# Kernel optimization log

Measured on AMD Instinct MI355X. Metric: run time of the kernel, lower is better.

The kernel has to match this reference:

```python
import jax, jax.numpy as jnp
import numpy as np

B, C, OC, H, W = 2, 64, 128, 96, 96
HD, DI, N, R, K = C // 2, C, 16, 2, 4  # VSSBlock: hidden=C/2, d_inner=2*hidden=C, d_state, dt_rank, 4 scan dirs
EPS = 1e-5


def _conv(x, w, b, pad, groups=1):
    y = jax.lax.conv_general_dilated(x, w, (1, 1), pad, feature_group_count=groups,
                                     dimension_numbers=('NCHW', 'OIHW', 'NCHW'))
    return y + b[None, :, None, None]


def _ln(x, w, b):
    m = x.mean(-1, keepdims=True)
    v = x.var(-1, keepdims=True)
    return (x - m) * jax.lax.rsqrt(v + EPS) * w + b


def _selective_scan(xs, dts, Bs, Cs, A, D):
    # xs, dts: (B,K,DI,L); Bs, Cs: (B,K,N,L); A: (K,DI,N); D: (K,DI)
    dts = jax.nn.softplus(dts)

    def step(h, inp):
        u_t, dt_t, B_t, C_t = inp
        dA = jnp.exp(dt_t[..., None] * A)                         # (B,K,DI,N)
        h = dA * h + (dt_t * u_t)[..., None] * B_t[:, :, None, :]
        return h, jnp.einsum('bkdn,bkn->bkd', h, C_t)

    seq = (jnp.moveaxis(xs, -1, 0), jnp.moveaxis(dts, -1, 0),
           jnp.moveaxis(Bs, -1, 0), jnp.moveaxis(Cs, -1, 0))
    h0 = jnp.zeros(xs.shape[:3] + (A.shape[-1],), xs.dtype)
    _, ys = jax.lax.scan(step, h0, seq)
    return jnp.moveaxis(ys, 0, -1) + D[None, :, :, None] * xs


def _vss_block(x, ln_w, ln_b, in_w, conv_w, conv_b, xproj_w, dtproj_w, dtproj_b,
               A_logs, Ds, on_w, on_b, out_w):
    # x: (B,H,W,HD); VMamba SS2D with 4-direction cross-scan + residual
    b, hh, ww, _ = x.shape
    L = hh * ww
    h = _ln(x, ln_w, ln_b)
    xz = h @ in_w                                   # (B,H,W,2*DI)
    xp, z = jnp.split(xz, 2, axis=-1)
    xc = jnp.transpose(xp, (0, 3, 1, 2))            # (B,DI,H,W)
    xc = jax.nn.silu(_conv(xc, conv_w, conv_b, ((1, 1), (1, 1)), groups=DI))
    x_flat = xc.reshape(b, DI, L)
    x_wh = jnp.transpose(xc, (0, 1, 3, 2)).reshape(b, DI, L)
    x2 = jnp.stack([x_flat, x_wh], axis=1)
    xs = jnp.concatenate([x2, jnp.flip(x2, -1)], axis=1)      # (B,4,DI,L)
    x_dbl = jnp.einsum('bkdl,kcd->bkcl', xs, xproj_w)
    dts, Bs, Cs = jnp.split(x_dbl, [R, R + N], axis=2)
    dts = jnp.einsum('bkrl,kdr->bkdl', dts, dtproj_w) + dtproj_b[None, :, :, None]
    A = -jnp.exp(A_logs)
    ys = _selective_scan(xs, dts, Bs, Cs, A, Ds)              # (B,4,DI,L)
    inv = jnp.flip(ys[:, 2:4], -1)
    unwh = lambda t: jnp.transpose(t.reshape(b, DI, ww, hh), (0, 1, 3, 2)).reshape(b, DI, L)
    y = ys[:, 0] + inv[:, 0] + unwh(ys[:, 1]) + unwh(inv[:, 1])
    y = jnp.transpose(y.reshape(b, DI, hh, ww), (0, 2, 3, 1))
    y = _ln(y, on_w, on_b) * jax.nn.silu(z)
    return x + y @ out_w


def _forward(x, ms_dw33_w, ms_dw33_b, ms_in_w, ms_in_b, ms_scale,
             vss_ln_w, vss_ln_b, vss_in_w, vss_conv_w, vss_conv_b, vss_xproj_w,
             vss_dtproj_w, vss_dtproj_b, vss_A_logs, vss_Ds, vss_on_w, vss_on_b, vss_out_w,
             ma_conv_w, ma_conv_b, adw_h_w, adw_h_b, adw_w_w, adw_w_b,
             pw_w, pw_b, bn_w, bn_b, bn_mean, bn_var):
    vss = (vss_ln_w, vss_ln_b, vss_in_w, vss_conv_w, vss_conv_b, vss_xproj_w,
           vss_dtproj_w, vss_dtproj_b, vss_A_logs, vss_Ds, vss_on_w, vss_on_b, vss_out_w)
    # --- MambaSplit (shared VSSBlock applied to both channel halves) ---
    xd = _conv(x, ms_dw33_w, ms_dw33_b, ((1, 1), (1, 1)), groups=C)
    x1, x2 = jnp.split(xd, 2, axis=1)

    def branch(xp):
        y = _vss_block(jnp.transpose(xp, (0, 2, 3, 1)), *vss)
        return ms_scale * xp + jnp.transpose(y, (0, 3, 1, 2))

    xm = jnp.concatenate([branch(x1), branch(x2)], axis=1)
    m = xm.mean((2, 3), keepdims=True)
    v = xm.var((2, 3), keepdims=True)
    xm = (xm - m) * jax.lax.rsqrt(v + EPS) * ms_in_w[None, :, None, None] + ms_in_b[None, :, None, None]
    xm = jax.nn.leaky_relu(xm, 0.01)
    # --- MaxAvg (global avg+max pool -> 3x3 conv on 1x1 map -> sigmoid gate) ---
    pooled = jnp.concatenate([x.mean((2, 3), keepdims=True), x.max((2, 3), keepdims=True)], axis=1)
    gate = jax.nn.sigmoid(_conv(pooled, ma_conv_w, ma_conv_b, ((1, 1), (1, 1))))
    xs_ = xm + gate * x
    # --- AxialDW ---
    xs_ = xs_ + _conv(xs_, adw_h_w, adw_h_b, ((1, 1), (0, 0)), groups=C) \
              + _conv(xs_, adw_w_w, adw_w_b, ((0, 0), (1, 1)), groups=C)
    # --- BN (eval) + ReLU, 1x1 conv, 2x2 maxpool ---
    skip = jax.nn.relu((xs_ - bn_mean[None, :, None, None]) * jax.lax.rsqrt(bn_var[None, :, None, None] + EPS)
                       * bn_w[None, :, None, None] + bn_b[None, :, None, None])
    out = _conv(skip, pw_w, pw_b, ((0, 0), (0, 0)))
    down = jax.lax.reduce_window(out, -jnp.inf, jax.lax.max, (1, 1, 2, 2), (1, 1, 2, 2), 'VALID')
    return down, skip


def setup_inputs() -> dict:
    key = jax.random.key(0)
    ks = jax.random.split(key, 16)
    r = lambda i, shape, s=0.02: jax.random.normal(ks[i], shape, jnp.float32) * s
    return {
        'x': jax.random.normal(ks[0], (B, C, H, W), jnp.float32),
        'ms_dw33_w': r(1, (C, 1, 3, 3), 0.1), 'ms_dw33_b': jnp.zeros(C),
        'ms_in_w': jnp.ones(C), 'ms_in_b': jnp.zeros(C),
        'ms_scale': jnp.ones((1,)),
        'vss_ln_w': jnp.ones(HD), 'vss_ln_b': jnp.zeros(HD),
        'vss_in_w': r(2, (HD, 2 * DI)),
        'vss_conv_w': r(3, (DI, 1, 3, 3), 0.1), 'vss_conv_b': jnp.zeros(DI),
        'vss_xproj_w': r(4, (K, R + 2 * N, DI)),
        'vss_dtproj_w': r(5, (K, DI, R), 0.1), 'vss_dtproj_b': r(6, (K, DI), 0.1),
        'vss_A_logs': jnp.tile(jnp.log(jnp.arange(1, N + 1, dtype=jnp.float32)), (K, DI, 1)),
        'vss_Ds': jnp.ones((K, DI)),
        'vss_on_w': jnp.ones(DI), 'vss_on_b': jnp.zeros(DI),
        'vss_out_w': r(7, (DI, HD)),
        'ma_conv_w': r(8, (C, 2 * C, 3, 3), 0.05), 'ma_conv_b': jnp.zeros(C),
        'adw_h_w': r(9, (C, 1, 3, 1), 0.1), 'adw_h_b': jnp.zeros(C),
        'adw_w_w': r(10, (C, 1, 1, 3), 0.1), 'adw_w_b': jnp.zeros(C),
        'pw_w': r(11, (OC, C, 1, 1)), 'pw_b': jnp.zeros(OC),
        'bn_w': jnp.ones(C), 'bn_b': jnp.zeros(C),
        'bn_mean': jnp.zeros(C), 'bn_var': jnp.ones(C),
    }


def reference(x, ms_dw33_w, ms_dw33_b, ms_in_w, ms_in_b, ms_scale,
              vss_ln_w, vss_ln_b, vss_in_w, vss_conv_w, vss_conv_b, vss_xproj_w,
              vss_dtproj_w, vss_dtproj_b, vss_A_logs, vss_Ds, vss_on_w, vss_on_b, vss_out_w,
              ma_conv_w, ma_conv_b, adw_h_w, adw_h_b, adw_w_w, adw_w_b,
              pw_w, pw_b, bn_w, bn_b, bn_mean, bn_var):
    return _forward(x, ms_dw33_w, ms_dw33_b, ms_in_w, ms_in_b, ms_scale,
                    vss_ln_w, vss_ln_b, vss_in_w, vss_conv_w, vss_conv_b, vss_xproj_w,
                    vss_dtproj_w, vss_dtproj_b, vss_A_logs, vss_Ds, vss_on_w, vss_on_b, vss_out_w,
                    ma_conv_w, ma_conv_b, adw_h_w, adw_h_b, adw_w_w, adw_w_b,
                    pw_w, pw_b, bn_w, bn_b, bn_mean, bn_var)
```

## Files before the change

kernel.cpp:

```cpp
#include <hip/hip_runtime.h>
#include <hip/hip_bf16.h>

typedef __hip_bfloat16 bf16;
#define DEV __device__ __forceinline__

constexpr int B_ = 2, C_ = 64, H_ = 96, W_ = 96, L_ = 9216;
constexpr int HD_ = 32, DI_ = 64, N_ = 16, K_ = 4, BB_ = 4;
constexpr int OC_ = 128;
constexpr int CH_ = 768, CL_ = 12;
constexpr int SEGN = 16, SEGC = 48;
constexpr float EPSF = 1e-5f;
constexpr int DOWN_SZ = B_ * OC_ * 48 * 48;

typedef __attribute__((ext_vector_type(8))) short short8;
typedef __attribute__((ext_vector_type(4))) float f32x4;

DEV float softplusf(float x) { return x > 15.f ? x : __logf(1.f + __expf(x)); }
DEV float b2f(bf16 v) { return __bfloat162float(v); }
DEV float lo16f(unsigned v) { return __uint_as_float(v << 16); }
DEV float hi16f(unsigned v) { return __uint_as_float(v & 0xffff0000u); }
DEV void unpk(uint4 a, uint4 b, float* v) {
  v[0] = lo16f(a.x); v[1] = hi16f(a.x); v[2] = lo16f(a.y); v[3] = hi16f(a.y);
  v[4] = lo16f(a.z); v[5] = hi16f(a.z); v[6] = lo16f(a.w); v[7] = hi16f(a.w);
  v[8] = lo16f(b.x); v[9] = hi16f(b.x); v[10] = lo16f(b.y); v[11] = hi16f(b.y);
  v[12] = lo16f(b.z); v[13] = hi16f(b.z); v[14] = lo16f(b.w); v[15] = hi16f(b.w);
}

__constant__ float kLogN[16] = {
  0.0f, 0.69314718f, 1.09861229f, 1.38629436f, 1.60943791f, 1.79175947f,
  1.94591015f, 2.07944154f, 2.19722458f, 2.30258509f, 2.39789527f,
  2.48490665f, 2.56494936f, 2.63905733f, 2.70805020f, 2.77258872f};

DEV void pow_tree(float e1, float* ep) {
  float e2 = e1 * e1, e4 = e2 * e2, e8 = e4 * e4;
  float e3 = e2 * e1, e5 = e4 * e1, e6 = e4 * e2, e7 = e4 * e3;
  ep[0] = e1;  ep[1] = e2;  ep[2] = e3;  ep[3] = e4;
  ep[4] = e5;  ep[5] = e6;  ep[6] = e7;  ep[7] = e8;
  ep[8] = e8 * e1;  ep[9] = e8 * e2;  ep[10] = e8 * e3;  ep[11] = e8 * e4;
  ep[12] = e8 * e5; ep[13] = e8 * e6; ep[14] = e8 * e7;  ep[15] = e8 * e8;
}

DEV void ld_bu(const float* __restrict__ bB, const bf16* __restrict__ ub, int d,
               int ls, int uidx, uint4& qb0, uint4& qb1, float& t0, float& t1, float& u) {
  int uls = __builtin_amdgcn_readfirstlane(ls);
  const float* p = bB + (size_t)uls * 12;
  qb0 = *(const uint4*)p; qb1 = *(const uint4*)(p + 4);
  t0 = p[8]; t1 = p[9];
  u = b2f(ub[(size_t)uidx * DI_ + d]);
}
DEV void ld_bcu(const float* __restrict__ bB, const bf16* __restrict__ bC,
                const bf16* __restrict__ ub, int d, int ls, int uidx,
                uint4& qb0, uint4& qb1, uint4& qc0, uint4& qc1,
                float& t0, float& t1, float& u) {
  int uls = __builtin_amdgcn_readfirstlane(ls);
  const float* p = bB + (size_t)uls * 12;
  qb0 = *(const uint4*)p; qb1 = *(const uint4*)(p + 4);
  t0 = p[8]; t1 = p[9];
  const uint4* cq = (const uint4*)(bC + (size_t)uls * 16);
  qc0 = cq[0]; qc1 = cq[1];
  u = b2f(ub[(size_t)uidx * DI_ + d]);
}

__global__ void k_dw33(const float* __restrict__ x, const float* __restrict__ w,
                       const float* __restrict__ bias, float* __restrict__ out) {
  int t = blockIdx.x * 256 + threadIdx.x;
  if (t >= B_ * C_ * L_) return;
  int wi = t % W_, hi = (t / W_) % H_, c = (t / L_) % C_;
  float acc = bias[c];
#pragma unroll
  for (int dy = -1; dy <= 1; dy++) {
    int hh = hi + dy; if (hh < 0 || hh >= H_) continue;
#pragma unroll
    for (int dx = -1; dx <= 1; dx++) {
      int ww = wi + dx; if (ww < 0 || ww >= W_) continue;
      acc = fmaf(x[t + dy * W_ + dx], w[c * 9 + (dy + 1) * 3 + (dx + 1)], acc);
    }
  }
  out[t] = acc;
}

__global__ __launch_bounds__(256, 4) void k_ln_inproj(
    const float* __restrict__ xd, const float* __restrict__ lnw,
    const float* __restrict__ lnb, const float* __restrict__ inw,
    float* __restrict__ xzA, bf16* __restrict__ xzBh) {
  int bb = blockIdx.y, t = threadIdx.x;
  int b = bb & 1, co = (bb >> 1) * HD_;
  int idx0 = blockIdx.x * 64;
  __shared__ float xds[32 * 68];
  __shared__ float meanA[64], rstdA[64];
  int lane = t & 63;
  for (int r = 0; r < 8; r++) {
    int c = r * 4 + (t >> 6);
    xds[c * 68 + lane] = xd[(size_t)(b * C_ + co + c) * L_ + idx0 + lane];
  }
  __syncthreads();
  if (t < 64) {
    float s = 0.f, sq = 0.f;
#pragma unroll
    for (int c = 0; c < 32; c++) { float v = xds[c * 68 + t]; s += v; sq = fmaf(v, v, sq); }
    float mean = s * (1.f / HD_);
    float var = sq * (1.f / HD_) - mean * mean;
    meanA[t] = mean; rstdA[t] = rsqrtf(var + EPSF);
  }
  __syncthreads();
  for (int i = t; i < 2048; i += 256) {
    int c = i >> 6, idx = i & 63;
    float v = xds[c * 68 + idx];
    xds[c * 68 + idx] = (v - meanA[idx]) * rstdA[idx] * lnw[c] + lnb[c];
  }
  __syncthreads();
  int oc = t & 127, g = t >> 7;
  float acc[32];
#pragma unroll
  for (int j = 0; j < 32; j++) acc[j] = 0.f;
  for (int c = 0; c < 32; c++) {
    float wv = inw[c * 128 + oc];
    const float4* row = reinterpret_cast<const float4*>(&xds[c * 68 + g * 32]);
#pragma unroll
    for (int j4 = 0; j4 < 8; j4++) {
      float4 xv = row[j4];
      acc[j4 * 4 + 0] = fmaf(xv.x, wv, acc[j4 * 4 + 0]);
      acc[j4 * 4 + 1] = fmaf(xv.y, wv, acc[j4 * 4 + 1]);
      acc[j4 * 4 + 2] = fmaf(xv.z, wv, acc[j4 * 4 + 2]);
      acc[j4 * 4 + 3] = fmaf(xv.w, wv, acc[j4 * 4 + 3]);
    }
  }
  int occ = oc & 63;
  if (oc < 64) {
#pragma unroll
    for (int j = 0; j < 32; j++)
      xzA[(size_t)(bb * L_ + idx0 + g * 32 + j) * 64 + occ] = acc[j];
  } else {
#pragma unroll
    for (int j = 0; j < 32; j++)
      xzBh[(size_t)(bb * L_ + idx0 + g * 32 + j) * 64 + occ] = __float2bfloat16(acc[j]);
  }
}

__global__ void k_dwsilu(const float* __restrict__ xzA, const float* __restrict__ cw,
                         const float* __restrict__ cb, bf16* __restrict__ xch,
                         bf16* __restrict__ xcht) {
  int t = blockIdx.x * 256 + threadIdx.x;
  int d = t & 63, idx = (t >> 6) % L_, bb = t / (L_ * DI_);
  int wi = idx % W_, hi = idx / W_;
  float acc = cb[d];
#pragma unroll
  for (int dy = -1; dy <= 1; dy++) {
    int hh = hi + dy; if (hh < 0 || hh >= H_) continue;
#pragma unroll
    for (int dx = -1; dx <= 1; dx++) {
      int ww = wi + dx; if (ww < 0 || ww >= W_) continue;
      acc = fmaf(xzA[(size_t)(bb * L_ + hh * W_ + ww) * 64 + d],
                 cw[d * 9 + (dy + 1) * 3 + (dx + 1)], acc);
    }
  }
  acc = acc / (1.f + __expf(-acc));
  bf16 v = __float2bfloat16(acc);
  xch[t] = v;
  int idx_t = wi * 96 + hi;
  xcht[((size_t)bb * L_ + idx_t) * DI_ + d] = v;
}

__global__ void k_wprep(const float* __restrict__ xpw, const float* __restrict__ alog,
                        bf16* __restrict__ wh, float* __restrict__ aux) {
  int i = blockIdx.x * 256 + threadIdx.x;
  if (i < 144 * 64) {
    int n = i >> 6;
    wh[i] = __float2bfloat16(n < 136 ? xpw[i] : 0.f);
  }
  if (blockIdx.x == 0 && threadIdx.x < 256) {
    int kd = threadIdx.x;
    const float* al = alog + kd * N_;
    float a0 = al[0];
    bool lin = true;
#pragma unroll
    for (int n = 1; n < N_; n++) lin = lin && (fabsf(al[n] - a0 - kLogN[n]) < 3e-5f);
    aux[kd] = -__expf(a0);
    aux[256 + kd] = lin ? 1.f : 0.f;
#pragma unroll
    for (int n = 0; n < N_; n++) aux[512 + kd * N_ + n] = -__expf(al[n]);
  }
}

__global__ __launch_bounds__(256, 4) void k_xdbl_mfma(
    const bf16* __restrict__ xch, const bf16* __restrict__ wh,
    float* __restrict__ xdblB, bf16* __restrict__ xdblC) {
  int w = threadIdx.x >> 6, lane = threadIdx.x & 63;
  int bb = blockIdx.y;
  int mtile = blockIdx.x * 4 + w;
  int idx0 = mtile * 16;
  int m = lane & 15, quad = lane >> 4;
  const bf16* arow = xch + ((size_t)bb * L_ + idx0 + m) * 64 + quad * 8;
  short8 a0 = *reinterpret_cast<const short8*>(arow);
  short8 a1 = *reinterpret_cast<const short8*>(arow + 32);
#pragma unroll
  for (int nt = 0; nt < 9; nt++) {
    int n = nt * 16 + m;
    const bf16* brow = wh + n * 64 + quad * 8;
    short8 b0 = *reinterpret_cast<const short8*>(brow);
    short8 b1 = *reinterpret_cast<const short8*>(brow + 32);
    f32x4 acc = {0.f, 0.f, 0.f, 0.f};
    acc = __builtin_amdgcn_mfma_f32_16x16x32_bf16(a0, b0, acc, 0, 0, 0);
    acc = __builtin_amdgcn_mfma_f32_16x16x32_bf16(a1, b1, acc, 0, 0, 0);
    if (n < 136) {
      int k4 = (n >= 102) ? 3 : (n >= 68) ? 2 : (n >= 34) ? 1 : 0;
      int c = n - k4 * 34;
#pragma unroll
      for (int i = 0; i < 4; i++) {
        int r = idx0 + quad * 4 + i;
        int hi2 = r / 96, wi2 = r - hi2 * 96;
        int tr = wi2 * 96 + hi2;
        int ls = (k4 == 0) ? r : (k4 == 1) ? tr : (k4 == 2) ? (L_ - 1 - r) : (L_ - 1 - tr);
        size_t row = (size_t)(bb * K_ + k4) * L_ + ls;
        if (c < 2)       xdblB[row * 12 + 8 + c] = acc[i];
        else if (c < 18) ((bf16*)(xdblB + row * 12))[c - 2] = __float2bfloat16(acc[i]);
        else             xdblC[row * 16 + (c - 18)] = __float2bfloat16(acc[i]);
      }
    }
  }
}

__global__ __launch_bounds__(256, 4) void k_scan1(
    const float* __restrict__ xdblB, const bf16* __restrict__ xch,
    const bf16* __restrict__ xcht, const float* __restrict__ dtw,
    const float* __restrict__ dtb, const float* __restrict__ aux,
    bf16* __restrict__ hbuf, float* __restrict__ ssum) {
  int w = threadIdx.x >> 6, d = threadIdx.x & 63;
  int chunk = blockIdx.x * 4 + w, k = blockIdx.y, bb = blockIdx.z;
  float w0 = dtw[(k * DI_ + d) * 2 + 0], w1 = dtw[(k * DI_ + d) * 2 + 1];
  float bia = dtb[k * DI_ + d];
  float A1 = aux[k * 64 + d];
  bool chain = (__ballot(aux[256 + k * 64 + d] > 0.5f) == ~0ull);
  float h[N_];
#pragma unroll
  for (int n = 0; n < N_; n++) h[n] = 0.f;
  const float* bB = xdblB + (size_t)(bb * K_ + k) * L_ * 12;
  const bf16* ub = ((k & 1) ? xcht : xch) + (size_t)bb * L_ * DI_;
  int ls0 = chunk * CL_;
  int uidx0 = (k & 2) ? (L_ - 1 - ls0) : ls0;
  int ustep = (k & 2) ? -1 : 1;
  float S = 0.f;
  if (chain) {
#pragma unroll 2
    for (int s = 0; s < CL_; s++) {
      uint4 qb0, qb1; float t0, t1, u;
      ld_bu(bB, ub, d, ls0 + s, uidx0 + s * ustep, qb0, qb1, t0, t1, u);
      float Bv[16];
      unpk(qb0, qb1, Bv);
      float dt = softplusf(fmaf(t0, w0, fmaf(t1, w1, bia)));
      S += dt;
      float du = dt * u;
      float ep[16];
      pow_tree(__expf(dt * A1), ep);
#pragma unroll
      for (int n = 0; n < N_; n++) h[n] = fmaf(ep[n], h[n], du * Bv[n]);
    }
  } else {
    float A[N_];
#pragma unroll
    for (int n = 0; n < N_; n++) A[n] = aux[512 + (k * 64 + d) * N_ + n];
    for (int s = 0; s < CL_; s++) {
      uint4 qb0, qb1; float t0, t1, u;
      ld_bu(bB, ub, d, ls0 + s, uidx0 + s * ustep, qb0, qb1, t0, t1, u);
      float Bv[16];
      unpk(qb0, qb1, Bv);
      float dt = softplusf(fmaf(t0, w0, fmaf(t1, w1, bia)));
      S += dt;
      float du = dt * u;
#pragma unroll
      for (int n = 0; n < N_; n++) h[n] = fmaf(__expf(dt * A[n]), h[n], du * Bv[n]);
    }
  }
  size_t base = (size_t)((bb * K_ + k) * CH_ + chunk) * DI_ + d;
  ssum[base] = S;
#pragma unroll
  for (int n = 0; n < N_; n++) hbuf[base * N_ + n] = __float2bfloat16(h[n]);
}

__global__ __launch_bounds__(256, 4) void k_scan2a(
    const float* __restrict__ aux, const float* __restrict__ ssum,
    bf16* __restrict__ hbuf, float* __restrict__ cumS,
    float* __restrict__ segH, float* __restrict__ segS) {
  int t = blockIdx.x * 256 + threadIdx.x;
  int n = t & 15, d = (t >> 4) & 63, kk = (t >> 10) & 3, bb = (t >> 12) & 3, seg = t >> 14;
  float A = aux[512 + (kk * 64 + d) * N_ + n];
  size_t row = (size_t)(bb * K_ + kk) * CH_ * DI_ + d;
  float hp = 0.f, Sc = 0.f;
#pragma unroll 4
  for (int j = 0; j < SEGC; j++) {
    int c = seg * SEGC + j;
    size_t sb = row + (size_t)c * DI_;
    float S = ssum[sb];
    float hl = b2f(hbuf[sb * N_ + n]);
    hbuf[sb * N_ + n] = __float2bfloat16(hp);
    if (n == 0) cumS[sb] = Sc;
    hp = fmaf(__expf(A * S), hp, hl);
    Sc += S;
  }
  size_t sbase = (size_t)(bb * K_ + kk) * SEGN + seg;
  segH[(sbase * DI_ + d) * N_ + n] = hp;
  if (n == 0) segS[sbase * DI_ + d] = Sc;
}

__global__ void k_scan2b(const float* __restrict__ aux, float* __restrict__ segH,
                         const float* __restrict__ segS) {
  int t = blockIdx.x * 256 + threadIdx.x;
  int n = t & 15, d = (t >> 4) & 63, kk = (t >> 10) & 3, bb = t >> 12;
  float A = aux[512 + (kk * 64 + d) * N_ + n];
  float hp = 0.f;
  for (int seg = 0; seg < SEGN; seg++) {
    size_t sbase = (size_t)(bb * K_ + kk) * SEGN + seg;
    size_t si = (sbase * DI_ + d) * N_ + n;
    float H = segH[si];
    float E = __expf(A * segS[sbase * DI_ + d]);
    segH[si] = hp;
    hp = fmaf(E, hp, H);
  }
}

__global__ __launch_bounds__(256, 4) void k_scan3(
    const float* __restrict__ xdblB, const bf16* __restrict__ xdblC,
    const bf16* __restrict__ xch, const bf16* __restrict__ xcht,
    const float* __restrict__ dtw, const float* __restrict__ dtb,
    const float* __restrict__ Dsw, const float* __restrict__ aux,
    const bf16* __restrict__ hbuf, const float* __restrict__ cumS,
    const float* __restrict__ segH, bf16* __restrict__ ydir) {
  int w = threadIdx.x >> 6, d = threadIdx.x & 63;
  int chunk = blockIdx.x * 4 + w, k = blockIdx.y, bb = blockIdx.z;
  float w0 = dtw[(k * DI_ + d) * 2 + 0], w1 = dtw[(k * DI_ + d) * 2 + 1];
  float bia = dtb[k * DI_ + d];
  float Dk = Dsw[k * DI_ + d];
  float A1 = aux[k * 64 + d];
  bool chain = (__ballot(aux[256 + k * 64 + d] > 0.5f) == ~0ull);
  float h[N_];
  size_t base = (size_t)((bb * K_ + k) * CH_ + chunk) * DI_ + d;
  int seg = chunk / SEGC;
  size_t sbase = (size_t)(bb * K_ + k) * SEGN + seg;
  float Sc = cumS[base];
  {
    const bf16* hb = hbuf + base * N_;
    uint4 qh0 = *(const uint4*)hb, qh1 = *(const uint4*)(hb + 8);
    unpk(qh0, qh1, h);
    const float* Hin = segH + (sbase * DI_ + d) * N_;
    if (chain) {
      float ep[16];
      pow_tree(__expf(A1 * Sc), ep);
#pragma unroll
      for (int n = 0; n < N_; n++) h[n] = fmaf(ep[n], Hin[n], h[n]);
    } else {
#pragma unroll
      for (int n = 0; n < N_; n++) {
        float A = aux[512 + (k * 64 + d) * N_ + n];
        h[n] = fmaf(__expf(A * Sc), Hin[n], h[n]);
      }
    }
  }
  const float* bB = xdblB + (size_t)(bb * K_ + k) * L_ * 12;
  const bf16* bC = xdblC + (size_t)(bb * K_ + k) * L_ * 16;
  const bf16* ub = ((k & 1) ? xcht : xch) + (size_t)bb * L_ * DI_;
  bf16* yb = ydir + (size_t)(bb * K_ + k) * L_ * DI_;
  int ls0 = chunk * CL_;
  int uidx0 = (k & 2) ? (L_ - 1 - ls0) : ls0;
  int ustep = (k & 2) ? -1 : 1;
  if (chain) {
#pragma unroll 2
    for (int s = 0; s < CL_; s++) {
      uint4 qb0, qb1, qc0, qc1; float t0, t1, u;
      ld_bcu(bB, bC, ub, d, ls0 + s, uidx0 + s * ustep, qb0, qb1, qc0, qc1, t0, t1, u);
      float Bv[16], Cv[16];
      unpk(qb0, qb1, Bv); unpk(qc0, qc1, Cv);
      float dt = softplusf(fmaf(t0, w0, fmaf(t1, w1, bia)));
      float du = dt * u;
      float ep[16];
      pow_tree(__expf(dt * A1), ep);
      float m[16];
#pragma unroll
      for (int n = 0; n < N_; n++) {
        h[n] = fmaf(ep[n], h[n], du * Bv[n]);
        m[n] = h[n] * Cv[n];
      }
      float a0 = m[0] + m[1], a1 = m[2] + m[3], a2 = m[4] + m[5], a3 = m[6] + m[7];
      float a4 = m[8] + m[9], a5 = m[10] + m[11], a6 = m[12] + m[13], a7 = m[14] + m[15];
      float b0 = a0 + a1, b1 = a2 + a3, b2 = a4 + a5, b3 = a6 + a7;
      float y = fmaf(Dk, u, (b0 + b1) + (b2 + b3));
      yb[(size_t)(ls0 + s) * DI_ + d] = __float2bfloat16(y);
    }
  } else {
    float A[N_];
#pragma unroll
    for (int n = 0; n < N_; n++) A[n] = aux[512 + (k * 64 + d) * N_ + n];
    for (int s = 0; s < CL_; s++) {
      uint4 qb0, qb1, qc0, qc1; float t0, t1, u;
      ld_bcu(bB, bC, ub, d, ls0 + s, uidx0 + s * ustep, qb0, qb1, qc0, qc1, t0, t1, u);
      float Bv[16], Cv[16];
      unpk(qb0, qb1, Bv); unpk(qc0, qc1, Cv);
      float dt = softplusf(fmaf(t0, w0, fmaf(t1, w1, bia)));
      float du = dt * u;
      float y = 0.f;
#pragma unroll
      for (int n = 0; n < N_; n++) {
        h[n] = fmaf(__expf(dt * A[n]), h[n], du * Bv[n]);
        y = fmaf(h[n], Cv[n], y);
      }
      y = fmaf(Dk, u, y);
      yb[(size_t)(ls0 + s) * DI_ + d] = __float2bfloat16(y);
    }
  }
}

__global__ void k_combine(const bf16* __restrict__ ydir, const bf16* __restrict__ xzBh,
                          const float* __restrict__ xd, const float* __restrict__ onw,
                          const float* __restrict__ onb, const float* __restrict__ outw,
                          const float* __restrict__ mssc, float* __restrict__ xm) {
  int w = threadIdx.x >> 6, d = threadIdx.x & 63;
  int idx = blockIdx.x * 4 + w, bb = blockIdx.y;
  int b = bb & 1, co = (bb >> 1) * HD_;
  int hii = idx / 96, wii = idx - hii * 96;
  int lt = wii * 96 + hii;
  const bf16* yd = ydir + (size_t)bb * K_ * L_ * DI_;
  float y = b2f(yd[((size_t)0 * L_ + idx) * DI_ + d])
          + b2f(yd[((size_t)1 * L_ + lt) * DI_ + d])
          + b2f(yd[((size_t)2 * L_ + (L_ - 1 - idx)) * DI_ + d])
          + b2f(yd[((size_t)3 * L_ + (L_ - 1 - lt)) * DI_ + d]);
  float s = y, sq = y * y;
#pragma unroll
  for (int m = 1; m < 64; m <<= 1) { s += __shfl_xor(s, m, 64); sq += __shfl_xor(sq, m, 64); }
  float mean = s * (1.f / DI_);
  float var = sq * (1.f / DI_) - mean * mean;
  float rstd = rsqrtf(var + EPSF);
  float yn = (y - mean) * rstd * onw[d] + onb[d];
  float z = b2f(xzBh[(size_t)(bb * L_ + idx) * 64 + d]);
  float g = yn * (z / (1.f + __expf(-z)));
  __shared__ float gs[4][DI_];
  gs[w][d] = g;
  __syncthreads();
  if (d < HD_) {
    float acc = 0.f;
#pragma unroll
    for (int dd = 0; dd < DI_; dd++) acc = fmaf(gs[w][dd], outw[dd * HD_ + d], acc);
    size_t xi = (size_t)(b * C_ + co + d) * L_ + idx;
    float xp = xd[xi];
    xm[xi] = mssc[0] * xp + xp + acc;
  }
}

__global__ __launch_bounds__(1024) void k_stats(
    const float* __restrict__ xm, const float* __restrict__ x,
    float* __restrict__ inm, float* __restrict__ inr,
    float* __restrict__ xmean, float* __restrict__ xmax) {
  int bc = blockIdx.x, t = threadIdx.x;
  const float* pm = xm + (size_t)bc * L_;
  const float* px = x + (size_t)bc * L_;
  float s = 0.f, sq = 0.f, xs = 0.f, mx = -1e30f;
  for (int i = t; i < L_; i += 1024) {
    float v = pm[i]; s += v; sq = fmaf(v, v, sq);
    float xv = px[i]; xs += xv; mx = fmaxf(mx, xv);
  }
  __shared__ float red[64];
#pragma unroll
  for (int m = 1; m < 64; m <<= 1) {
    s += __shfl_xor(s, m, 64); sq += __shfl_xor(sq, m, 64);
    xs += __shfl_xor(xs, m, 64); mx = fmaxf(mx, __shfl_xor(mx, m, 64));
  }
  int wid = t >> 6;
  if ((t & 63) == 0) { red[wid] = s; red[16 + wid] = sq; red[32 + wid] = xs; red[48 + wid] = mx; }
  __syncthreads();
  if (t == 0) {
    s = 0.f; sq = 0.f; xs = 0.f; mx = -1e30f;
#pragma unroll
    for (int i = 0; i < 16; i++) {
      s += red[i]; sq += red[16 + i]; xs += red[32 + i]; mx = fmaxf(mx, red[48 + i]);
    }
    float mean = s * (1.f / L_);
    float var = sq * (1.f / L_) - mean * mean;
    inm[bc] = mean;
    inr[bc] = rsqrtf(var + EPSF);
    xmean[bc] = xs * (1.f / L_);
    xmax[bc] = mx;
  }
}

__global__ void k_xs(const float* __restrict__ xm, const float* __restrict__ inm,
                     const float* __restrict__ inr, const float* __restrict__ msw,
                     const float* __restrict__ msb, const float* __restrict__ xmean,
                     const float* __restrict__ xmax, const float* __restrict__ maw,
                     const float* __restrict__ mab, const float* __restrict__ x,
                     float* __restrict__ xs2) {
  int t = blockIdx.x * 256 + threadIdx.x;
  int bc = t / L_, c = bc & 63, b = bc >> 6;
  __shared__ float gsh;
  if (threadIdx.x < 64) {
    int ic = threadIdx.x;
    float p = xmean[b * 64 + ic] * maw[(c * 128 + ic) * 9 + 4]
            + xmax[b * 64 + ic] * maw[(c * 128 + 64 + ic) * 9 + 4];
#pragma unroll
    for (int m = 1; m < 64; m <<= 1) p += __shfl_xor(p, m, 64);
    if (ic == 0) gsh = 1.f / (1.f + __expf(-(p + mab[c])));
  }
  __syncthreads();
  float gate = gsh;
  float v = xm[t];
  v = (v - inm[bc]) * inr[bc] * msw[c] + msb[c];
  v = v > 0.f ? v : 0.01f * v;
  xs2[t] = v + gate * x[t];
}

__global__ void k_axbn(const float* __restrict__ xs2, const float* __restrict__ hw,
                       const float* __restrict__ hb, const float* __restrict__ wwt,
                       const float* __restrict__ wb, const float* __restrict__ bnw,
                       const float* __restrict__ bnb, const float* __restrict__ bnm,
                       const float* __restrict__ bnv, float* __restrict__ skipo) {
  int t = blockIdx.x * 256 + threadIdx.x;
  if (t >= B_ * C_ * L_) return;
  int wi = t % W_, hi = (t / W_) % H_, c = (t / L_) % C_;
  float a = xs2[t];
  float hacc = hb[c];
#pragma unroll
  for (int dy = -1; dy <= 1; dy++) {
    int hh = hi + dy; if (hh < 0 || hh >= H_) continue;
    hacc = fmaf(xs2[t + dy * W_], hw[c * 3 + dy + 1], hacc);
  }
  float wacc = wb[c];
#pragma unroll
  for (int dx = -1; dx <= 1; dx++) {
    int ww = wi + dx; if (ww < 0 || ww >= W_) continue;
    wacc = fmaf(xs2[t + dx], wwt[c * 3 + dx + 1], wacc);
  }
  float v = a + hacc + wacc;
  float sv = (v - bnm[c]) * rsqrtf(bnv[c] + EPSF) * bnw[c] + bnb[c];
  skipo[t] = fmaxf(sv, 0.f);
}

__global__ void k_pwpool(const float* __restrict__ skipo, const float* __restrict__ pww,
                         const float* __restrict__ pwb, float* __restrict__ down) {
  int h2 = blockIdx.x, b = blockIdx.y, t = threadIdx.x;
  int oc0 = blockIdx.z * 32;
  __shared__ float sk[64 * 192];
  for (int i = t; i < 64 * 192; i += 256) {
    int c = i / 192, rw = i % 192, r = rw / 96, wcol = rw % 96;
    sk[i] = skipo[((size_t)(b * C_ + c) * H_ + (2 * h2 + r)) * W_ + wcol];
  }
  __syncthreads();
  for (int o = t; o < 32 * 48; o += 256) {
    int oc = oc0 + o / 48, w2 = o % 48;
    float s0 = 0.f, s1 = 0.f, s2 = 0.f, s3 = 0.f;
#pragma unroll 8
    for (int c = 0; c < 64; c++) {
      float wv = pww[oc * 64 + c];
      const float* sp = &sk[c * 192 + 2 * w2];
      s0 = fmaf(sp[0], wv, s0);
      s1 = fmaf(sp[1], wv, s1);
      s2 = fmaf(sp[96], wv, s2);
      s3 = fmaf(sp[97], wv, s3);
    }
    float v = fmaxf(fmaxf(s0, s1), fmaxf(s2, s3)) + pwb[oc];
    down[((size_t)(b * OC_ + oc) * 48 + h2) * 48 + w2] = v;
  }
}

extern "C" void kernel_launch(void* const* d_in, const int* in_sizes, int n_in,
                              void* d_out, int out_size, void* d_ws, size_t ws_size,
                              hipStream_t stream) {
  const float* x     = (const float*)d_in[0];
  const float* dw33w = (const float*)d_in[1];
  const float* dw33b = (const float*)d_in[2];
  const float* msw   = (const float*)d_in[3];
  const float* msb   = (const float*)d_in[4];
  const float* mssc  = (const float*)d_in[5];
  const float* lnw   = (const float*)d_in[6];
  const float* lnb   = (const float*)d_in[7];
  const float* inw   = (const float*)d_in[8];
  const float* cw    = (const float*)d_in[9];
  const float* cb    = (const float*)d_in[10];
  const float* xpw   = (const float*)d_in[11];
  const float* dtw   = (const float*)d_in[12];
  const float* dtb   = (const float*)d_in[13];
  const float* alog  = (const float*)d_in[14];
  const float* Dsw   = (const float*)d_in[15];
  const float* onw   = (const float*)d_in[16];
  const float* onb   = (const float*)d_in[17];
  const float* outw  = (const float*)d_in[18];
  const float* maw   = (const float*)d_in[19];
  const float* mab   = (const float*)d_in[20];
  const float* ahw   = (const float*)d_in[21];
  const float* ahb   = (const float*)d_in[22];
  const float* aww   = (const float*)d_in[23];
  const float* awb   = (const float*)d_in[24];
  const float* pww   = (const float*)d_in[25];
  const float* pwb   = (const float*)d_in[26];
  const float* bnw   = (const float*)d_in[27];
  const float* bnb   = (const float*)d_in[28];
  const float* bnm   = (const float*)d_in[29];
  const float* bnv   = (const float*)d_in[30];

  float* ws = (float*)d_ws;
  float* xd    = ws;
  float* hreg  = xd + 1179648;
  bf16*  hbuf  = (bf16*)hreg;
  float* xzA   = hreg;
  bf16*  xzBh  = (bf16*)(hreg + 6291456);
  float* xdblB = hreg + 6291456 + 1179648;
  bf16*  xdblC = (bf16*)(xdblB + 1769472);
  float* ssum  = xdblB + 1769472 + 1179648;
  bf16*  ydir  = (bf16*)(ssum + 786432);
  float* xmR   = ssum + 786432 + 4718592;
  bf16*  xch   = (bf16*)xmR;
  float* xm    = xmR;
  float* xs2   = (float*)ydir;
  float* st    = xmR + 1179648;
  float* inm = st, *inr = st + 128, *xmean = st + 256, *xmaxv = st + 384;
  float* aux   = st + 512;
  bf16*  wh    = (bf16*)(aux + 4608);
  float* cumS  = aux + 4608 + 4608;
  float* segH  = cumS + 786432;
  float* segS  = segH + 262144;
  bf16*  xcht  = (bf16*)(segS + 16384);

  float* outp = (float*)d_out;
  float* down = outp;
  float* skipo = outp + DOWN_SZ;

  dim3 b256(256);
  int nEl = B_ * C_ * L_;

  k_wprep<<<dim3(36), b256, 0, stream>>>(xpw, alog, wh, aux);
  k_dw33<<<dim3((nEl + 255) / 256), b256, 0, stream>>>(x, dw33w, dw33b, xd);
  k_ln_inproj<<<dim3(L_ / 64, BB_), b256, 0, stream>>>(xd, lnw, lnb, inw, xzA, xzBh);
  k_dwsilu<<<dim3(BB_ * L_ * DI_ / 256), b256, 0, stream>>>(xzA, cw, cb, xch, xcht);
  k_xdbl_mfma<<<dim3(L_ / 64, BB_), b256, 0, stream>>>(xch, wh, xdblB, xdblC);
  k_scan1<<<dim3(CH_ / 4, K_, BB_), b256, 0, stream>>>(xdblB, xch, xcht, dtw, dtb, aux, hbuf, ssum);
  k_scan2a<<<dim3(BB_ * K_ * SEGN * DI_ * N_ / 256), b256, 0, stream>>>(aux, ssum, hbuf, cumS, segH, segS);
  k_scan2b<<<dim3(BB_ * K_ * DI_ * N_ / 256), b256, 0, stream>>>(aux, segH, segS);
  k_scan3<<<dim3(CH_ / 4, K_, BB_), b256, 0, stream>>>(xdblB, xdblC, xch, xcht, dtw, dtb, Dsw,
                                                      aux, hbuf, cumS, segH, ydir);
  k_combine<<<dim3(L_ / 4, BB_), b256, 0, stream>>>(ydir, xzBh, xd, onw, onb, outw, mssc, xm);
  k_stats<<<dim3(B_ * C_), dim3(1024), 0, stream>>>(xm, x, inm, inr, xmean, xmaxv);
  k_xs<<<dim3((nEl + 255) / 256), b256, 0, stream>>>(xm, inm, inr, msw, msb, xmean, xmaxv, maw, mab, x, xs2);
  k_axbn<<<dim3((nEl + 255) / 256), b256, 0, stream>>>(xs2, ahw, ahb, aww, awb, bnw, bnb, bnm, bnv, skipo);
  k_pwpool<<<dim3(48, B_, 4), b256, 0, stream>>>(skipo, pww, pwb, down);
}
```

Baseline: 320.7 us.

## Fuse front-end kernels, fold segment-carry scan into scan3, merge xs into axbn

Merges weight prep, the depthwise 3x3 conv and LayerNorm+in-proj into a single front kernel that computes the conv directly into shared memory. Removes the separate cross-segment scan kernel by having each scan3 thread recompute its segment-prefix state from segH/segS. Fuses the xs computation into the axial-conv+BN kernel, recomputing neighbour values instead of round-tripping xs2 through memory. Intent is fewer launches and less intermediate global traffic, at the cost of redundant recomputation.

```diff
diff --git a/kernel.cpp b/kernel.cpp
--- a/kernel.cpp
+++ b/kernel.cpp
@@ -61,37 +61,54 @@
   u = b2f(ub[(size_t)uidx * DI_ + d]);
 }
 
-__global__ void k_dw33(const float* __restrict__ x, const float* __restrict__ w,
-                       const float* __restrict__ bias, float* __restrict__ out) {
-  int t = blockIdx.x * 256 + threadIdx.x;
-  if (t >= B_ * C_ * L_) return;
-  int wi = t % W_, hi = (t / W_) % H_, c = (t / L_) % C_;
-  float acc = bias[c];
-#pragma unroll
-  for (int dy = -1; dy <= 1; dy++) {
-    int hh = hi + dy; if (hh < 0 || hh >= H_) continue;
-#pragma unroll
-    for (int dx = -1; dx <= 1; dx++) {
-      int ww = wi + dx; if (ww < 0 || ww >= W_) continue;
-      acc = fmaf(x[t + dy * W_ + dx], w[c * 9 + (dy + 1) * 3 + (dx + 1)], acc);
-    }
-  }
-  out[t] = acc;
-}
-
-__global__ __launch_bounds__(256, 4) void k_ln_inproj(
-    const float* __restrict__ xd, const float* __restrict__ lnw,
+__global__ __launch_bounds__(256, 4) void k_front(
+    const float* __restrict__ x, const float* __restrict__ dw33w,
+    const float* __restrict__ dw33b, const float* __restrict__ lnw,
     const float* __restrict__ lnb, const float* __restrict__ inw,
-    float* __restrict__ xzA, bf16* __restrict__ xzBh) {
+    const float* __restrict__ xpw, const float* __restrict__ alog,
+    float* __restrict__ xd, float* __restrict__ xzA, bf16* __restrict__ xzBh,
+    bf16* __restrict__ wh, float* __restrict__ aux) {
   int bb = blockIdx.y, t = threadIdx.x;
   int b = bb & 1, co = (bb >> 1) * HD_;
   int idx0 = blockIdx.x * 64;
+  if (bb == 0) {
+    int i = blockIdx.x * 256 + t;
+    if (i < 144 * 64) {
+      int n = i >> 6;
+      wh[i] = __float2bfloat16(n < 136 ? xpw[i] : 0.f);
+    }
+    if (blockIdx.x == 0) {
+      int kd = t;
+      const float* al = alog + kd * N_;
+      float a0 = al[0];
+      bool lin = true;
+#pragma unroll
+      for (int n = 1; n < N_; n++) lin = lin && (fabsf(al[n] - a0 - kLogN[n]) < 3e-5f);
+      aux[kd] = -__expf(a0);
+      aux[256 + kd] = lin ? 1.f : 0.f;
+#pragma unroll
+      for (int n = 0; n < N_; n++) aux[512 + kd * N_ + n] = -__expf(al[n]);
+    }
+  }
   __shared__ float xds[32 * 68];
   __shared__ float meanA[64], rstdA[64];
-  int lane = t & 63;
-  for (int r = 0; r < 8; r++) {
-    int c = r * 4 + (t >> 6);
-    xds[c * 68 + lane] = xd[(size_t)(b * C_ + co + c) * L_ + idx0 + lane];
+  for (int i = t; i < 2048; i += 256) {
+    int cl = i >> 6, ii = i & 63;
+    int sp = idx0 + ii, wi = sp % 96, hi = sp / 96;
+    int cg = b * C_ + co + cl;
+    float acc = dw33b[co + cl];
+#pragma unroll
+    for (int dy = -1; dy <= 1; dy++) {
+      int hh = hi + dy; if (hh < 0 || hh >= H_) continue;
+#pragma unroll
+      for (int dx = -1; dx <= 1; dx++) {
+        int ww = wi + dx; if (ww < 0 || ww >= W_) continue;
+        acc = fmaf(x[(size_t)cg * L_ + sp + dy * 96 + dx],
+                   dw33w[(co + cl) * 9 + (dy + 1) * 3 + (dx + 1)], acc);
+      }
+    }
+    xds[cl * 68 + ii] = acc;
+    xd[(size_t)cg * L_ + sp] = acc;
   }
   __syncthreads();
   if (t < 64) {
@@ -159,27 +176,6 @@
   xch[t] = v;
   int idx_t = wi * 96 + hi;
   xcht[((size_t)bb * L_ + idx_t) * DI_ + d] = v;
-}
-
-__global__ void k_wprep(const float* __restrict__ xpw, const float* __restrict__ alog,
-                        bf16* __restrict__ wh, float* __restrict__ aux) {
-  int i = blockIdx.x * 256 + threadIdx.x;
-  if (i < 144 * 64) {
-    int n = i >> 6;
-    wh[i] = __float2bfloat16(n < 136 ? xpw[i] : 0.f);
-  }
-  if (blockIdx.x == 0 && threadIdx.x < 256) {
-    int kd = threadIdx.x;
-    const float* al = alog + kd * N_;
-    float a0 = al[0];
-    bool lin = true;
-#pragma unroll
-    for (int n = 1; n < N_; n++) lin = lin && (fabsf(al[n] - a0 - kLogN[n]) < 3e-5f);
-    aux[kd] = -__expf(a0);
-    aux[256 + kd] = lin ? 1.f : 0.f;
-#pragma unroll
-    for (int n = 0; n < N_; n++) aux[512 + kd * N_ + n] = -__expf(al[n]);
-  }
 }
 
 __global__ __launch_bounds__(256, 4) void k_xdbl_mfma(
@@ -302,29 +298,14 @@
   if (n == 0) segS[sbase * DI_ + d] = Sc;
 }
 
-__global__ void k_scan2b(const float* __restrict__ aux, float* __restrict__ segH,
-                         const float* __restrict__ segS) {
-  int t = blockIdx.x * 256 + threadIdx.x;
-  int n = t & 15, d = (t >> 4) & 63, kk = (t >> 10) & 3, bb = t >> 12;
-  float A = aux[512 + (kk * 64 + d) * N_ + n];
-  float hp = 0.f;
-  for (int seg = 0; seg < SEGN; seg++) {
-    size_t sbase = (size_t)(bb * K_ + kk) * SEGN + seg;
-    size_t si = (sbase * DI_ + d) * N_ + n;
-    float H = segH[si];
-    float E = __expf(A * segS[sbase * DI_ + d]);
-    segH[si] = hp;
-    hp = fmaf(E, hp, H);
-  }
-}
-
 __global__ __launch_bounds__(256, 4) void k_scan3(
     const float* __restrict__ xdblB, const bf16* __restrict__ xdblC,
     const bf16* __restrict__ xch, const bf16* __restrict__ xcht,
     const float* __restrict__ dtw, const float* __restrict__ dtb,
     const float* __restrict__ Dsw, const float* __restrict__ aux,
     const bf16* __restrict__ hbuf, const float* __restrict__ cumS,
-    const float* __restrict__ segH, bf16* __restrict__ ydir) {
+    const float* __restrict__ segH, const float* __restrict__ segS,
+    bf16* __restrict__ ydir) {
   int w = threadIdx.x >> 6, d = threadIdx.x & 63;
   int chunk = blockIdx.x * 4 + w, k = blockIdx.y, bb = blockIdx.z;
   float w0 = dtw[(k * DI_ + d) * 2 + 0], w1 = dtw[(k * DI_ + d) * 2 + 1];
@@ -332,27 +313,44 @@
   float Dk = Dsw[k * DI_ + d];
   float A1 = aux[k * 64 + d];
   bool chain = (__ballot(aux[256 + k * 64 + d] > 0.5f) == ~0ull);
+  float A[N_];
+  if (!chain) {
+#pragma unroll
+    for (int n = 0; n < N_; n++) A[n] = aux[512 + (k * 64 + d) * N_ + n];
+  }
+  int seg = chunk / SEGC;
+  float Hi[N_];
+#pragma unroll
+  for (int n = 0; n < N_; n++) Hi[n] = 0.f;
+  for (int s = 0; s < seg; s++) {
+    size_t sb = (size_t)(bb * K_ + k) * SEGN + s;
+    float Ssg = segS[sb * DI_ + d];
+    const float* Hs = segH + (sb * DI_ + d) * N_;
+    if (chain) {
+      float ep[16];
+      pow_tree(__expf(A1 * Ssg), ep);
+#pragma unroll
+      for (int n = 0; n < N_; n++) Hi[n] = fmaf(ep[n], Hi[n], Hs[n]);
+    } else {
+#pragma unroll
+      for (int n = 0; n < N_; n++) Hi[n] = fmaf(__expf(A[n] * Ssg), Hi[n], Hs[n]);
+    }
+  }
   float h[N_];
   size_t base = (size_t)((bb * K_ + k) * CH_ + chunk) * DI_ + d;
-  int seg = chunk / SEGC;
-  size_t sbase = (size_t)(bb * K_ + k) * SEGN + seg;
   float Sc = cumS[base];
   {
     const bf16* hb = hbuf + base * N_;
     uint4 qh0 = *(const uint4*)hb, qh1 = *(const uint4*)(hb + 8);
     unpk(qh0, qh1, h);
-    const float* Hin = segH + (sbase * DI_ + d) * N_;
     if (chain) {
       float ep[16];
       pow_tree(__expf(A1 * Sc), ep);
 #pragma unroll
-      for (int n = 0; n < N_; n++) h[n] = fmaf(ep[n], Hin[n], h[n]);
+      for (int n = 0; n < N_; n++) h[n] = fmaf(ep[n], Hi[n], h[n]);
     } else {
 #pragma unroll
-      for (int n = 0; n < N_; n++) {
-        float A = aux[512 + (k * 64 + d) * N_ + n];
-        h[n] = fmaf(__expf(A * Sc), Hin[n], h[n]);
-      }
+      for (int n = 0; n < N_; n++) h[n] = fmaf(__expf(A[n] * Sc), Hi[n], h[n]);
     }
   }
   const float* bB = xdblB + (size_t)(bb * K_ + k) * L_ * 12;
@@ -386,9 +384,6 @@
       yb[(size_t)(ls0 + s) * DI_ + d] = __float2bfloat16(y);
     }
   } else {
-    float A[N_];
-#pragma unroll
-    for (int n = 0; n < N_; n++) A[n] = aux[512 + (k * 64 + d) * N_ + n];
     for (int s = 0; s < CL_; s++) {
       uint4 qb0, qb1, qc0, qc1; float t0, t1, u;
       ld_bcu(bB, bC, ub, d, ls0 + s, uidx0 + s * ustep, qb0, qb1, qc0, qc1, t0, t1, u);
@@ -480,12 +475,16 @@
   }
 }
 
-__global__ void k_xs(const float* __restrict__ xm, const float* __restrict__ inm,
-                     const float* __restrict__ inr, const float* __restrict__ msw,
-                     const float* __restrict__ msb, const float* __restrict__ xmean,
-                     const float* __restrict__ xmax, const float* __restrict__ maw,
-                     const float* __restrict__ mab, const float* __restrict__ x,
-                     float* __restrict__ xs2) {
+__global__ void k_axbn(const float* __restrict__ xm, const float* __restrict__ x,
+                       const float* __restrict__ inm, const float* __restrict__ inr,
+                       const float* __restrict__ msw, const float* __restrict__ msb,
+                       const float* __restrict__ xmean, const float* __restrict__ xmax,
+                       const float* __restrict__ maw, const float* __restrict__ mab,
+                       const float* __restrict__ hw, const float* __restrict__ hb,
+                       const float* __restrict__ wwt, const float* __restrict__ wb,
+                       const float* __restrict__ bnw, const float* __restrict__ bnb,
+                       const float* __restrict__ bnm, const float* __restrict__ bnv,
+                       float* __restrict__ skipo) {
   int t = blockIdx.x * 256 + threadIdx.x;
   int bc = t / L_, c = bc & 63, b = bc >> 6;
   __shared__ float gsh;
@@ -498,33 +497,26 @@
     if (ic == 0) gsh = 1.f / (1.f + __expf(-(p + mab[c])));
   }
   __syncthreads();
-  float gate = gsh;
-  float v = xm[t];
-  v = (v - inm[bc]) * inr[bc] * msw[c] + msb[c];
-  v = v > 0.f ? v : 0.01f * v;
-  xs2[t] = v + gate * x[t];
-}
-
-__global__ void k_axbn(const float* __restrict__ xs2, const float* __restrict__ hw,
-                       const float* __restrict__ hb, const float* __restrict__ wwt,
-                       const float* __restrict__ wb, const float* __restrict__ bnw,
-                       const float* __restrict__ bnb, const float* __restrict__ bnm,
-                       const float* __restrict__ bnv, float* __restrict__ skipo) {
-  int t = blockIdx.x * 256 + threadIdx.x;
-  if (t >= B_ * C_ * L_) return;
-  int wi = t % W_, hi = (t / W_) % H_, c = (t / L_) % C_;
-  float a = xs2[t];
+  float gate = gsh, im = inm[bc], ir = inr[bc], mw = msw[c], mb = msb[c];
+  int wi = t % W_, hi = (t / W_) % H_;
+  auto xsv = [&](int tt) -> float {
+    float v = xm[tt];
+    v = (v - im) * ir * mw + mb;
+    v = v > 0.f ? v : 0.01f * v;
+    return v + gate * x[tt];
+  };
+  float a = xsv(t);
   float hacc = hb[c];
 #pragma unroll
   for (int dy = -1; dy <= 1; dy++) {
     int hh = hi + dy; if (hh < 0 || hh >= H_) continue;
-    hacc = fmaf(xs2[t + dy * W_], hw[c * 3 + dy + 1], hacc);
+    hacc = fmaf(xsv(t + dy * W_), hw[c * 3 + dy + 1], hacc);
   }
   float wacc = wb[c];
 #pragma unroll
   for (int dx = -1; dx <= 1; dx++) {
     int ww = wi + dx; if (ww < 0 || ww >= W_) continue;
-    wacc = fmaf(xs2[t + dx], wwt[c * 3 + dx + 1], wacc);
+    wacc = fmaf(xsv(t + dx), wwt[c * 3 + dx + 1], wacc);
   }
   float v = a + hacc + wacc;
   float sv = (v - bnm[c]) * rsqrtf(bnv[c] + EPSF) * bnw[c] + bnb[c];
@@ -606,7 +598,6 @@
   float* xmR   = ssum + 786432 + 4718592;
   bf16*  xch   = (bf16*)xmR;
   float* xm    = xmR;
-  float* xs2   = (float*)ydir;
   float* st    = xmR + 1179648;
   float* inm = st, *inr = st + 128, *xmean = st + 256, *xmaxv = st + 384;
   float* aux   = st + 512;
@@ -623,19 +614,18 @@
   dim3 b256(256);
   int nEl = B_ * C_ * L_;
 
-  k_wprep<<<dim3(36), b256, 0, stream>>>(xpw, alog, wh, aux);
-  k_dw33<<<dim3((nEl + 255) / 256), b256, 0, stream>>>(x, dw33w, dw33b, xd);
-  k_ln_inproj<<<dim3(L_ / 64, BB_), b256, 0, stream>>>(xd, lnw, lnb, inw, xzA, xzBh);
+  k_front<<<dim3(L_ / 64, BB_), b256, 0, stream>>>(x, dw33w, dw33b, lnw, lnb, inw,
+                                                   xpw, alog, xd, xzA, xzBh, wh, aux);
   k_dwsilu<<<dim3(BB_ * L_ * DI_ / 256), b256, 0, stream>>>(xzA, cw, cb, xch, xcht);
   k_xdbl_mfma<<<dim3(L_ / 64, BB_), b256, 0, stream>>>(xch, wh, xdblB, xdblC);
   k_scan1<<<dim3(CH_ / 4, K_, BB_), b256, 0, stream>>>(xdblB, xch, xcht, dtw, dtb, aux, hbuf, ssum);
   k_scan2a<<<dim3(BB_ * K_ * SEGN * DI_ * N_ / 256), b256, 0, stream>>>(aux, ssum, hbuf, cumS, segH, segS);
-  k_scan2b<<<dim3(BB_ * K_ * DI_ * N_ / 256), b256, 0, stream>>>(aux, segH, segS);
   k_scan3<<<dim3(CH_ / 4, K_, BB_), b256, 0, stream>>>(xdblB, xdblC, xch, xcht, dtw, dtb, Dsw,
-                                                      aux, hbuf, cumS, segH, ydir);
+                                                      aux, hbuf, cumS, segH, segS, ydir);
   k_combine<<<dim3(L_ / 4, BB_), b256, 0, stream>>>(ydir, xzBh, xd, onw, onb, outw, mssc, xm);
   k_stats<<<dim3(B_ * C_), dim3(1024), 0, stream>>>(xm, x, inm, inr, xmean, xmaxv);
-  k_xs<<<dim3((nEl + 255) / 256), b256, 0, stream>>>(xm, inm, inr, msw, msb, xmean, xmaxv, maw, mab, x, xs2);
-  k_axbn<<<dim3((nEl + 255) / 256), b256, 0, stream>>>(xs2, ahw, ahb, aww, awb, bnw, bnb, bnm, bnv, skipo);
+  k_axbn<<<dim3((nEl + 255) / 256), b256, 0, stream>>>(xm, x, inm, inr, msw, msb, xmean, xmaxv,
+                                                      maw, mab, ahw, ahb, aww, awb,
+                                                      bnw, bnb, bnm, bnv, skipo);
   k_pwpool<<<dim3(48, B_, 4), b256, 0, stream>>>(skipo, pww, pwb, down);
 }
```

New measurement: 343.7 us. 1.07x slower.
